# Performance work log

Hardware: AMD Instinct MI355X
Metric: run time of the kernel (lower is better)

## Reference

```python
import math
import jax, jax.numpy as jnp
import numpy as np

N_HEADS = 16
NUM_BUCKETS = 32
MAX_DISTANCE = 128


def _relative_position_bucket(relative_positions, num_buckets=NUM_BUCKETS, max_distance=MAX_DISTANCE):
    # bidirectional=True branch of the torch helper
    ret = -relative_positions
    nb = num_buckets // 2
    sign = (ret < 0).astype(jnp.int32)
    ret = jnp.abs(ret)
    max_exact = nb // 2
    is_small = ret < max_exact
    # torch .long() truncates toward zero; values in the selected (large) branch are >= 0 so int cast matches
    large = max_exact + jnp.minimum(
        (jnp.log(ret.astype(jnp.float32) / max_exact + 1e-6)
         / math.log(max_distance / max_exact) * (nb - max_exact)).astype(jnp.int32),
        nb - max_exact - 1,
    )
    return jnp.where(is_small, ret, large) + sign * nb


def setup_inputs() -> dict:
    key = jax.random.key(0)
    k1, k2, k3, k4, k5 = jax.random.split(key, 5)
    d_model = 1024
    B, L = 2, 2048
    return {
        "query": jax.random.normal(k1, (B, L, d_model), dtype=jnp.float32),
        "Wq": jax.random.normal(k2, (d_model, d_model), dtype=jnp.float32) * 0.02,
        "Wkv": jax.random.normal(k3, (d_model, 2 * d_model), dtype=jnp.float32) * 0.02,
        "Wo": jax.random.normal(k4, (d_model, d_model), dtype=jnp.float32) * 0.02,
        "rel_bias": jax.random.normal(k5, (N_HEADS * NUM_BUCKETS, 1), dtype=jnp.float32) * 0.02,
    }


def reference(query, Wq, Wkv, Wo, rel_bias):
    B, L, D = query.shape
    H = N_HEADS
    hd = D // H
    scale = 1.0 / math.sqrt(hd)

    q = query @ Wq                      # [B, L, D]
    kv = query @ Wkv                    # [B, L, 2D]
    k, v = jnp.split(kv, 2, axis=-1)

    def split_heads(x):
        return x.reshape(B, L, H, hd).transpose(0, 2, 1, 3)  # [B, H, L, hd]

    q, k, v = map(split_heads, (q, k, v))

    scores = jnp.einsum("bhqd,bhkd->bhqk", q, k) * scale      # [B, H, L, L]

    # relative position bias
    pos = jnp.arange(L)
    rp = pos[None, :] - pos[:, None]                           # mem - ctx, [L, L]
    buckets = _relative_position_bucket(rp)                    # [L, L]
    idx = buckets[None, :, :] + (jnp.arange(H) * NUM_BUCKETS)[:, None, None]  # [H, L, L]
    bias = rel_bias[idx, 0][None]                              # [1, H, L, L]

    attn = jax.nn.softmax(scores + bias, axis=-1)
    out = jnp.einsum("bhqk,bhkd->bhqd", attn, v)               # [B, H, L, hd]
    out = out.transpose(0, 2, 1, 3).reshape(B, L, D) @ Wo      # [B, L, D]
    return out, bias
```

## Files before the change

### kernel.cpp

```cpp
#include <hip/hip_runtime.h>


typedef unsigned short u16;
typedef unsigned int u32;
typedef __attribute__((ext_vector_type(4))) float f32x4;
typedef __attribute__((ext_vector_type(8))) short bf16x8;
typedef __attribute__((ext_vector_type(4))) unsigned short u16x4;

#define MFMA16(a, b, c) __builtin_amdgcn_mfma_f32_16x16x32_bf16(a, b, c, 0, 0, 0)

typedef const __attribute__((address_space(1))) void gvoid;
typedef __attribute__((address_space(3))) void lvoid;
static __device__ __forceinline__ void gll16(const void* g, void* l) {
    __builtin_amdgcn_global_load_lds((gvoid*)g, (lvoid*)l, 16, 0, 0);
}

static __device__ inline u16 f2bf(float f) {
    u32 x = __float_as_uint(f);
    x += 0x7fffu + ((x >> 16) & 1u);
    return (u16)(x >> 16);
}
static __device__ inline u32 pk2(float a, float b) {
    return (u32)f2bf(a) | ((u32)f2bf(b) << 16);
}

__global__ __launch_bounds__(256) void prep(
    const float* __restrict__ X, const float* __restrict__ Wq,
    const float* __restrict__ Wkv, const float* __restrict__ Wo,
    const float* __restrict__ rel_bias, u16* __restrict__ Xb,
    u16* __restrict__ Wt, float* __restrict__ tbl)
{
    __shared__ u16 T[64 * 72];
    const int bx = blockIdx.x, tid = threadIdx.x;
    if (bx < 2048) {
        int i = (bx * 256 + tid) * 8;
        float4 a = *(const float4*)(X + i);
        float4 b = *(const float4*)(X + i + 4);
        uint4 w = { pk2(a.x, a.y), pk2(a.z, a.w), pk2(b.x, b.y), pk2(b.z, b.w) };
        *(uint4*)(Xb + i) = w;
    } else if (bx < 3072) {
        int bx2 = bx - 2048;
        int k0 = (bx2 & 15) * 64;
        int n0 = (bx2 >> 4) * 64;
        const float* src; int ld, nb;
        if (n0 < 1024)      { src = Wq;  ld = 1024; nb = n0; }
        else if (n0 < 3072) { src = Wkv; ld = 2048; nb = n0 - 1024; }
        else                { src = Wo;  ld = 1024; nb = n0 - 3072; }
        const int r0 = tid >> 4, c4 = (tid & 15) * 4;
        for (int rr = 0; rr < 4; rr++) {
            int row = rr * 16 + r0;
            float4 f = *(const float4*)(src + (size_t)(k0 + row) * ld + nb + c4);
            T[(c4 + 0) * 72 + row] = f2bf(f.x);
            T[(c4 + 1) * 72 + row] = f2bf(f.y);
            T[(c4 + 2) * 72 + row] = f2bf(f.z);
            T[(c4 + 3) * 72 + row] = f2bf(f.w);
        }
        __syncthreads();
        const int n = tid >> 2, ks0 = (tid & 3) * 16;
        uint4 u0 = *(const uint4*)&T[n * 72 + ks0];
        uint4 u1 = *(const uint4*)&T[n * 72 + ks0 + 8];
        uint4* d = (uint4*)(Wt + (size_t)(n0 + n) * 1024 + k0 + ks0);
        d[0] = u0; d[1] = u1;
    } else {
        int i = (bx - 3072) * 256 + tid;
        int rel = (i & 4095) - 2047;
        int h = i >> 12;
        int ret = -rel;
        int sign = (ret < 0) ? 1 : 0;
        int aret = (ret < 0) ? -ret : ret;
        int bucket;
        if (aret < 8) {
            bucket = aret;
        } else {
            float v = (logf((float)aret * 0.125f + 1e-6f) / logf(16.0f)) * 8.0f;
            int iv = (int)v;
            bucket = 8 + (iv < 7 ? iv : 7);
        }
        bucket += sign * 16;
        tbl[i] = rel_bias[h * 32 + bucket];
    }
}

__global__ __launch_bounds__(256) void qkv_gemm(
    const u16* __restrict__ Xb, const u16* __restrict__ Wt,
    u16* __restrict__ qws, u16* __restrict__ kws, u16* __restrict__ vtws)
{
    __shared__ u16 As[128 * 64];
    __shared__ u16 Bs[128 * 64];
    const int tid = threadIdx.x;
    const int n0 = blockIdx.x * 128;
    const int m0 = blockIdx.y * 128;
    const int wid = tid >> 6, lane = tid & 63, c = lane & 15, quad = lane >> 4;
    const int wm = (wid >> 1) * 64, wn = (wid & 1) * 64;
    const f32x4 z = {0.f, 0.f, 0.f, 0.f};
    f32x4 acc[4][4];
    for (int i = 0; i < 4; i++) for (int j = 0; j < 4; j++) acc[i][j] = z;
    const int rsub = lane >> 3;
    const int dchunk = (lane & 7) ^ (rsub & 7);
    const u16* ag = Xb + (size_t)(m0 + wid * 32 + rsub) * 1024 + dchunk * 8;
    const u16* bg = Wt + (size_t)(n0 + wid * 32 + rsub) * 1024 + dchunk * 8;
    u16* lA = &As[(wid * 32) * 64];
    u16* lB = &Bs[(wid * 32) * 64];
    const int sw = c & 7;

    for (int kk = 0; kk < 1024; kk += 64) {
        for (int i = 0; i < 4; i++)
            gll16(ag + (size_t)i * 8 * 1024 + kk, lA + i * 8 * 64);
        for (int i = 0; i < 4; i++)
            gll16(bg + (size_t)i * 8 * 1024 + kk, lB + i * 8 * 64);
        __syncthreads();
        for (int ks = 0; ks < 2; ks++) {
            const int sl = ((ks * 4 + quad) ^ sw) * 8;
            bf16x8 af[4], bfr[4];
            for (int im = 0; im < 4; im++)
                af[im] = *(const bf16x8*)&As[(wm + im * 16 + c) * 64 + sl];
            for (int jn = 0; jn < 4; jn++)
                bfr[jn] = *(const bf16x8*)&Bs[(wn + jn * 16 + c) * 64 + sl];
            for (int im = 0; im < 4; im++)
                for (int jn = 0; jn < 4; jn++)
                    acc[im][jn] = MFMA16(af[im], bfr[jn], acc[im][jn]);
        }
        __syncthreads();
    }
    for (int im = 0; im < 4; im++) for (int jn = 0; jn < 4; jn++) {
        int gm0 = m0 + wm + im * 16 + quad * 4;
        int gn = n0 + wn + jn * 16 + c;
        if (gn < 2048) {
            u16* dstbase = (gn < 1024) ? qws : kws;
            int nn = gn & 1023;
            int h = nn >> 6, d = nn & 63;
            for (int r = 0; r < 4; r++) {
                int gm = gm0 + r, bb = gm >> 11, l = gm & 2047;
                dstbase[(((size_t)bb * 16 + h) * 2048 + l) * 64 + d] = f2bf(acc[im][jn][r]);
            }
        } else {
            int nn = gn - 2048;
            int h = nn >> 6, d = nn & 63;
            int bb = gm0 >> 11, l = gm0 & 2047;
            u16x4 pk = { f2bf(acc[im][jn][0]), f2bf(acc[im][jn][1]),
                         f2bf(acc[im][jn][2]), f2bf(acc[im][jn][3]) };
            *(u16x4*)&vtws[(((size_t)bb * 16 + h) * 64 + d) * 2048 + l] = pk;
        }
    }
}

__global__ __launch_bounds__(256, 2) void attn_kernel(
    const u16* __restrict__ qws, const u16* __restrict__ kws,
    const u16* __restrict__ vtws, const float* __restrict__ tbl,
    u16* __restrict__ ows, float* __restrict__ bias_out)
{
    __shared__ u16 QPs[128 * 72];
    __shared__ u16 Ks[2][64 * 72];
    __shared__ u16 Vt[2][64 * 72];
    __shared__ float Bw[2][192];
    const int tid = threadIdx.x;
    const int qt = blockIdx.x, bh = blockIdx.y;
    const int b = bh >> 4, h = bh & 15;
    const u16* qp = qws + (size_t)bh * 2048 * 64;
    const u16* kp = kws + (size_t)bh * 2048 * 64;
    const u16* vp = vtws + (size_t)bh * 64 * 2048;
    const float* tb = tbl + h * 4096;
    const int q0 = qt * 128;
    const int wid = tid >> 6, lane = tid & 63, c = lane & 15, quad = lane >> 4;
    const int qw0 = wid * 32;
    const int srow = tid >> 2, sc0 = (tid & 3) * 16;
    const int birow = tid >> 3, bjj = (tid & 7) * 4;

    {
        int row = tid >> 1, c0 = (tid & 1) * 32;
        const uint4* s = (const uint4*)(qp + (size_t)(q0 + row) * 64 + c0);
        uint4 v0 = s[0], v1 = s[1], v2 = s[2], v3 = s[3];
        uint4* d = (uint4*)&QPs[row * 72 + c0];
        d[0] = v0; d[1] = v1; d[2] = v2; d[3] = v3;
    }
    {
        const uint4* s1 = (const uint4*)(kp + (size_t)srow * 64 + sc0);
        uint4 x0 = s1[0], x1 = s1[1];
        const uint4* s2 = (const uint4*)(vp + (size_t)srow * 2048 + sc0);
        uint4 y0 = s2[0], y1 = s2[1];
        *(uint4*)&Ks[0][srow * 72 + sc0] = x0;
        *(uint4*)&Ks[0][srow * 72 + sc0 + 8] = x1;
        *(uint4*)&Vt[0][srow * 72 + sc0] = y0;
        *(uint4*)&Vt[0][srow * 72 + sc0 + 8] = y1;
        if (tid < 192) Bw[0][tid] = tb[1920 - q0 + tid];
    }
    __syncthreads();
    bf16x8 bq[2][2];
    for (int nt = 0; nt < 2; nt++)
        for (int ks = 0; ks < 2; ks++)
            bq[nt][ks] = *(const bf16x8*)&QPs[(qw0 + nt * 16 + c) * 72 + ks * 32 + quad * 8];
    __syncthreads();
    u16* Ps = QPs + wid * (32 * 72);

    float lrow[2] = { 0.f, 0.f };
    const f32x4 z = {0.f, 0.f, 0.f, 0.f};
    f32x4 accO[2][4];
    for (int i = 0; i < 2; i++) for (int j = 0; j < 4; j++) accO[i][j] = z;

    for (int kt = 0; kt < 32; kt++) {
        const int cur = kt & 1, nxt = cur ^ 1;
        const int k0 = kt * 64;
        uint4 x0, x1, y0, y1; float bwv = 0.f;
        if (kt < 31) {
            const uint4* s1 = (const uint4*)(kp + (size_t)(k0 + 64 + srow) * 64 + sc0);
            x0 = s1[0]; x1 = s1[1];
            const uint4* s2 = (const uint4*)(vp + (size_t)srow * 2048 + k0 + 64 + sc0);
            y0 = s2[0]; y1 = s2[1];
            if (tid < 192) bwv = tb[k0 + 64 - q0 + 1920 + tid];
        }
        f32x4 accS[4][2];
        for (int i = 0; i < 4; i++) { accS[i][0] = z; accS[i][1] = z; }
        for (int ks = 0; ks < 2; ks++)
            for (int ktile = 0; ktile < 4; ktile++) {
                bf16x8 ak = *(const bf16x8*)&Ks[cur][(ktile * 16 + c) * 72 + ks * 32 + quad * 8];
                accS[ktile][0] = MFMA16(ak, bq[0][ks], accS[ktile][0]);
                accS[ktile][1] = MFMA16(ak, bq[1][ks], accS[ktile][1]);
            }
        float rsum[2] = { 0.f, 0.f };
        for (int ktile = 0; ktile < 4; ktile++)
            for (int nt = 0; nt < 2; nt++) {
                const float* bp = &Bw[cur][ktile * 16 + quad * 4 - qw0 - nt * 16 - c + 127];
                float p0 = __expf(fmaf(accS[ktile][nt][0], 0.125f, bp[0]));
                float p1 = __expf(fmaf(accS[ktile][nt][1], 0.125f, bp[1]));
                float p2 = __expf(fmaf(accS[ktile][nt][2], 0.125f, bp[2]));
                float p3 = __expf(fmaf(accS[ktile][nt][3], 0.125f, bp[3]));
                rsum[nt] += (p0 + p1) + (p2 + p3);
                u16x4 pk = { f2bf(p0), f2bf(p1), f2bf(p2), f2bf(p3) };
                *(u16x4*)&Ps[(nt * 16 + c) * 72 + ktile * 16 + quad * 4] = pk;
            }
        lrow[0] += rsum[0]; lrow[1] += rsum[1];
        for (int kb = 0; kb < 2; kb++) {
            bf16x8 bv[4];
            for (int nt = 0; nt < 4; nt++)
                bv[nt] = *(const bf16x8*)&Vt[cur][(nt * 16 + c) * 72 + kb * 32 + quad * 8];
            for (int mt = 0; mt < 2; mt++) {
                bf16x8 ap = *(const bf16x8*)&Ps[(mt * 16 + c) * 72 + kb * 32 + quad * 8];
                for (int nt = 0; nt < 4; nt++)
                    accO[mt][nt] = MFMA16(ap, bv[nt], accO[mt][nt]);
            }
        }
        {
            const int jbase = k0 + b * 32 + bjj;
            const float* tw = tb + (jbase + 2047 - q0);
            float* dstb = bias_out + ((size_t)h * 2048 + q0 + birow) * 2048 + jbase;
            for (int rr = 0; rr < 4; rr++) {
                const float* twp = tw - (birow + rr * 32);
                f32x4 v = { twp[0], twp[1], twp[2], twp[3] };
                __builtin_nontemporal_store(v, (f32x4*)(dstb + (size_t)rr * 32 * 2048));
            }
        }
        if (kt < 31) {
            *(uint4*)&Ks[nxt][srow * 72 + sc0] = x0;
            *(uint4*)&Ks[nxt][srow * 72 + sc0 + 8] = x1;
            *(uint4*)&Vt[nxt][srow * 72 + sc0] = y0;
            *(uint4*)&Vt[nxt][srow * 72 + sc0 + 8] = y1;
            if (tid < 192) Bw[nxt][tid] = bwv;
            __syncthreads();
        }
    }
    for (int nt = 0; nt < 2; nt++) {
        lrow[nt] += __shfl_xor(lrow[nt], 16, 64);
        lrow[nt] += __shfl_xor(lrow[nt], 32, 64);
    }
    for (int mt = 0; mt < 2; mt++)
        for (int r = 0; r < 4; r++) {
            float lq = __shfl(lrow[mt], quad * 4 + r, 64);
            float rl = 1.0f / lq;
            int qg = q0 + qw0 + mt * 16 + quad * 4 + r;
            size_t base = ((size_t)b * 2048 + qg) * 1024 + h * 64;
            for (int nt = 0; nt < 4; nt++)
                ows[base + nt * 16 + c] = f2bf(accO[mt][nt][r] * rl);
        }
}

__global__ __launch_bounds__(256) void out_gemm(
    const u16* __restrict__ O, const u16* __restrict__ Wot, float* __restrict__ out)
{
    __shared__ u16 As[128 * 64];
    __shared__ u16 Bs[128 * 64];
    const int tid = threadIdx.x;
    const int n0 = blockIdx.x * 128;
    const int m0 = blockIdx.y * 128;
    const int wid = tid >> 6, lane = tid & 63, c = lane & 15, quad = lane >> 4;
    const int wm = (wid >> 1) * 64, wn = (wid & 1) * 64;
    const f32x4 z = {0.f, 0.f, 0.f, 0.f};
    f32x4 acc[4][4];
    for (int i = 0; i < 4; i++) for (int j = 0; j < 4; j++) acc[i][j] = z;
    const int rsub = lane >> 3;
    const int dchunk = (lane & 7) ^ (rsub & 7);
    const u16* ag = O + (size_t)(m0 + wid * 32 + rsub) * 1024 + dchunk * 8;
    const u16* bg = Wot + (size_t)(n0 + wid * 32 + rsub) * 1024 + dchunk * 8;
    u16* lA = &As[(wid * 32) * 64];
    u16* lB = &Bs[(wid * 32) * 64];
    const int sw = c & 7;
    for (int kk = 0; kk < 1024; kk += 64) {
        for (int i = 0; i < 4; i++)
            gll16(ag + (size_t)i * 8 * 1024 + kk, lA + i * 8 * 64);
        for (int i = 0; i < 4; i++)
            gll16(bg + (size_t)i * 8 * 1024 + kk, lB + i * 8 * 64);
        __syncthreads();
        for (int ks = 0; ks < 2; ks++) {
            const int sl = ((ks * 4 + quad) ^ sw) * 8;
            bf16x8 af[4], bfr[4];
            for (int im = 0; im < 4; im++)
                af[im] = *(const bf16x8*)&As[(wm + im * 16 + c) * 64 + sl];
            for (int jn = 0; jn < 4; jn++)
                bfr[jn] = *(const bf16x8*)&Bs[(wn + jn * 16 + c) * 64 + sl];
            for (int im = 0; im < 4; im++)
                for (int jn = 0; jn < 4; jn++)
                    acc[im][jn] = MFMA16(af[im], bfr[jn], acc[im][jn]);
        }
        __syncthreads();
    }
    for (int im = 0; im < 4; im++) for (int jn = 0; jn < 4; jn++) {
        int gm0 = m0 + wm + im * 16 + quad * 4;
        int gn = n0 + wn + jn * 16 + c;
        for (int r = 0; r < 4; r++)
            __builtin_nontemporal_store(acc[im][jn][r], &out[(size_t)(gm0 + r) * 1024 + gn]);
    }
}

extern "C" void kernel_launch(void* const* d_in, const int* in_sizes, int n_in,
                              void* d_out, int out_size, void* d_ws, size_t ws_size,
                              hipStream_t stream)
{
    (void)in_sizes; (void)n_in; (void)out_size; (void)ws_size;
    const float* query    = (const float*)d_in[0];
    const float* Wq       = (const float*)d_in[1];
    const float* Wkv      = (const float*)d_in[2];
    const float* Wo       = (const float*)d_in[3];
    const float* rel_bias = (const float*)d_in[4];
    float* out = (float*)d_out;

    float* tbl = (float*)d_ws;
    u16* Xb   = (u16*)((char*)d_ws + 262144);
    u16* Wt   = Xb + 4194304;
    u16* qws  = Wt + 4194304;
    u16* kws  = qws + 4194304;
    u16* vtws = kws + 4194304;
    u16* ows  = vtws + 4194304;

    prep<<<3328, 256, 0, stream>>>(query, Wq, Wkv, Wo, rel_bias, Xb, Wt, tbl);
    qkv_gemm<<<dim3(24, 32), 256, 0, stream>>>(Xb, Wt, qws, kws, vtws);
    attn_kernel<<<dim3(16, 32), 256, 0, stream>>>(qws, kws, vtws, tbl, ows,
                                                  out + 4194304);
    out_gemm<<<dim3(8, 32), 256, 0, stream>>>(ows, Wt + (size_t)3072 * 1024, out);
}
```

Measured before the change: 401.7 us.

## Stage K/V tiles with direct global-to-LDS loads into XOR-swizzled layout

Replaces the register-staged K and V tile prefetch with global_load_lds 16-byte transfers straight into shared memory. The padded row stride of 72 becomes an unpadded stride of 64 with an XOR swizzle on the 8-element chunk index to avoid bank conflicts. The bias tile is premultiplied by log2(e) and the score scale adjusted so exp2f can replace __expf. The aim is to cut VGPR pressure and the register round-trip for prefetch, but it relies on the sync at the end of each iteration to order async LDS writes against reads.

```diff
diff --git a/kernel.cpp b/kernel.cpp
--- a/kernel.cpp
+++ b/kernel.cpp
@@ -150,8 +150,8 @@
     u16* __restrict__ ows, float* __restrict__ bias_out)
 {
     __shared__ u16 QPs[128 * 72];
-    __shared__ u16 Ks[2][64 * 72];
-    __shared__ u16 Vt[2][64 * 72];
+    __shared__ u16 Ks[2][64 * 64];
+    __shared__ u16 Vt[2][64 * 64];
     __shared__ float Bw[2][192];
     const int tid = threadIdx.x;
     const int qt = blockIdx.x, bh = blockIdx.y;
@@ -163,26 +163,28 @@
     const int q0 = qt * 128;
     const int wid = tid >> 6, lane = tid & 63, c = lane & 15, quad = lane >> 4;
     const int qw0 = wid * 32;
-    const int srow = tid >> 2, sc0 = (tid & 3) * 16;
+    const int sw = c & 7;
+    const int rsub = lane >> 3;
+    const int schunk = (lane & 7) ^ rsub;
     const int birow = tid >> 3, bjj = (tid & 7) * 4;
 
+    auto stage = [&](int buf, int k0) {
+        for (int g = 0; g < 2; g++) {
+            gll16(kp + (size_t)(k0 + wid * 16 + g * 8 + rsub) * 64 + schunk * 8,
+                  &Ks[buf][(wid * 16 + g * 8) * 64]);
+            gll16(vp + (size_t)(wid * 16 + g * 8 + rsub) * 2048 + k0 + schunk * 8,
+                  &Vt[buf][(wid * 16 + g * 8) * 64]);
+        }
+        if (tid < 192) Bw[buf][tid] = tb[k0 - q0 + 1920 + tid] * 1.44269504f;
+    };
+
+    stage(0, 0);
     {
         int row = tid >> 1, c0 = (tid & 1) * 32;
         const uint4* s = (const uint4*)(qp + (size_t)(q0 + row) * 64 + c0);
         uint4 v0 = s[0], v1 = s[1], v2 = s[2], v3 = s[3];
         uint4* d = (uint4*)&QPs[row * 72 + c0];
         d[0] = v0; d[1] = v1; d[2] = v2; d[3] = v3;
-    }
-    {
-        const uint4* s1 = (const uint4*)(kp + (size_t)srow * 64 + sc0);
-        uint4 x0 = s1[0], x1 = s1[1];
-        const uint4* s2 = (const uint4*)(vp + (size_t)srow * 2048 + sc0);
-        uint4 y0 = s2[0], y1 = s2[1];
-        *(uint4*)&Ks[0][srow * 72 + sc0] = x0;
-        *(uint4*)&Ks[0][srow * 72 + sc0 + 8] = x1;
-        *(uint4*)&Vt[0][srow * 72 + sc0] = y0;
-        *(uint4*)&Vt[0][srow * 72 + sc0 + 8] = y1;
-        if (tid < 192) Bw[0][tid] = tb[1920 - q0 + tid];
     }
     __syncthreads();
     bf16x8 bq[2][2];
@@ -198,21 +200,15 @@
     for (int i = 0; i < 2; i++) for (int j = 0; j < 4; j++) accO[i][j] = z;
 
     for (int kt = 0; kt < 32; kt++) {
-        const int cur = kt & 1, nxt = cur ^ 1;
+        const int cur = kt & 1;
         const int k0 = kt * 64;
-        uint4 x0, x1, y0, y1; float bwv = 0.f;
-        if (kt < 31) {
-            const uint4* s1 = (const uint4*)(kp + (size_t)(k0 + 64 + srow) * 64 + sc0);
-            x0 = s1[0]; x1 = s1[1];
-            const uint4* s2 = (const uint4*)(vp + (size_t)srow * 2048 + k0 + 64 + sc0);
-            y0 = s2[0]; y1 = s2[1];
-            if (tid < 192) bwv = tb[k0 + 64 - q0 + 1920 + tid];
-        }
+        if (kt < 31) stage(cur ^ 1, k0 + 64);
         f32x4 accS[4][2];
         for (int i = 0; i < 4; i++) { accS[i][0] = z; accS[i][1] = z; }
         for (int ks = 0; ks < 2; ks++)
             for (int ktile = 0; ktile < 4; ktile++) {
-                bf16x8 ak = *(const bf16x8*)&Ks[cur][(ktile * 16 + c) * 72 + ks * 32 + quad * 8];
+                bf16x8 ak = *(const bf16x8*)
+                    &Ks[cur][(ktile * 16 + c) * 64 + (((ks * 4 + quad) ^ sw)) * 8];
                 accS[ktile][0] = MFMA16(ak, bq[0][ks], accS[ktile][0]);
                 accS[ktile][1] = MFMA16(ak, bq[1][ks], accS[ktile][1]);
             }
@@ -220,10 +216,10 @@
         for (int ktile = 0; ktile < 4; ktile++)
             for (int nt = 0; nt < 2; nt++) {
                 const float* bp = &Bw[cur][ktile * 16 + quad * 4 - qw0 - nt * 16 - c + 127];
-                float p0 = __expf(fmaf(accS[ktile][nt][0], 0.125f, bp[0]));
-                float p1 = __expf(fmaf(accS[ktile][nt][1], 0.125f, bp[1]));
-                float p2 = __expf(fmaf(accS[ktile][nt][2], 0.125f, bp[2]));
-                float p3 = __expf(fmaf(accS[ktile][nt][3], 0.125f, bp[3]));
+                float p0 = exp2f(fmaf(accS[ktile][nt][0], 0.180336878f, bp[0]));
+                float p1 = exp2f(fmaf(accS[ktile][nt][1], 0.180336878f, bp[1]));
+                float p2 = exp2f(fmaf(accS[ktile][nt][2], 0.180336878f, bp[2]));
+                float p3 = exp2f(fmaf(accS[ktile][nt][3], 0.180336878f, bp[3]));
                 rsum[nt] += (p0 + p1) + (p2 + p3);
                 u16x4 pk = { f2bf(p0), f2bf(p1), f2bf(p2), f2bf(p3) };
                 *(u16x4*)&Ps[(nt * 16 + c) * 72 + ktile * 16 + quad * 4] = pk;
@@ -232,7 +228,8 @@
         for (int kb = 0; kb < 2; kb++) {
             bf16x8 bv[4];
             for (int nt = 0; nt < 4; nt++)
-                bv[nt] = *(const bf16x8*)&Vt[cur][(nt * 16 + c) * 72 + kb * 32 + quad * 8];
+                bv[nt] = *(const bf16x8*)
+                    &Vt[cur][(nt * 16 + c) * 64 + (((kb * 4 + quad) ^ sw)) * 8];
             for (int mt = 0; mt < 2; mt++) {
                 bf16x8 ap = *(const bf16x8*)&Ps[(mt * 16 + c) * 72 + kb * 32 + quad * 8];
                 for (int nt = 0; nt < 4; nt++)
@@ -249,14 +246,7 @@
                 __builtin_nontemporal_store(v, (f32x4*)(dstb + (size_t)rr * 32 * 2048));
             }
         }
-        if (kt < 31) {
-            *(uint4*)&Ks[nxt][srow * 72 + sc0] = x0;
-            *(uint4*)&Ks[nxt][srow * 72 + sc0 + 8] = x1;
-            *(uint4*)&Vt[nxt][srow * 72 + sc0] = y0;
-            *(uint4*)&Vt[nxt][srow * 72 + sc0 + 8] = y1;
-            if (tid < 192) Bw[nxt][tid] = bwv;
-            __syncthreads();
-        }
+        __syncthreads();
     }
     for (int nt = 0; nt < 2; nt++) {
         lrow[nt] += __shfl_xor(lrow[nt], 16, 64);
```

Result: no change. 405.6 us (+1.0%).

## Split bias tensor writes between QKV GEMM and attention; use exp2 softmax

Applied to the files above, without the earlier changes.

Half of the large relative-position bias output (alternate 64-column groups) is now written by the QKV GEMM kernel, interleaved with its K loop, so those stores overlap GEMM compute. The attention kernel writes only the remaining half. The softmax switches from expf to exp2f by pre-scaling the bias and the score scale by log2(e), which removes a multiply per exponent. The risk is extra memory traffic contending with the GEMM's global-to-LDS loads. A no-op change to the swizzle expression is also included.

```diff
diff --git a/kernel.cpp b/kernel.cpp
--- a/kernel.cpp
+++ b/kernel.cpp
@@ -83,7 +83,8 @@
 
 __global__ __launch_bounds__(256) void qkv_gemm(
     const u16* __restrict__ Xb, const u16* __restrict__ Wt,
-    u16* __restrict__ qws, u16* __restrict__ kws, u16* __restrict__ vtws)
+    u16* __restrict__ qws, u16* __restrict__ kws, u16* __restrict__ vtws,
+    const float* __restrict__ tbl, float* __restrict__ bias_out)
 {
     __shared__ u16 As[128 * 64];
     __shared__ u16 Bs[128 * 64];
@@ -96,14 +97,16 @@
     f32x4 acc[4][4];
     for (int i = 0; i < 4; i++) for (int j = 0; j < 4; j++) acc[i][j] = z;
     const int rsub = lane >> 3;
-    const int dchunk = (lane & 7) ^ (rsub & 7);
+    const int dchunk = (lane & 7) ^ rsub;
     const u16* ag = Xb + (size_t)(m0 + wid * 32 + rsub) * 1024 + dchunk * 8;
     const u16* bg = Wt + (size_t)(n0 + wid * 32 + rsub) * 1024 + dchunk * 8;
     u16* lA = &As[(wid * 32) * 64];
     u16* lB = &Bs[(wid * 32) * 64];
     const int sw = c & 7;
-
-    for (int kk = 0; kk < 1024; kk += 64) {
+    const u32 bl = blockIdx.y * 24 + blockIdx.x;
+
+    for (int it = 0; it < 16; it++) {
+        const int kk = it * 64;
         for (int i = 0; i < 4; i++)
             gll16(ag + (size_t)i * 8 * 1024 + kk, lA + i * 8 * 64);
         for (int i = 0; i < 4; i++)
@@ -119,6 +122,22 @@
             for (int im = 0; im < 4; im++)
                 for (int jn = 0; jn < 4; jn++)
                     acc[im][jn] = MFMA16(af[im], bfr[jn], acc[im][jn]);
+        }
+        {
+            const u32 fbase = ((bl * 16 + (u32)it) * 256 + (u32)tid) * 3;
+            for (u32 t = 0; t < 3; t++) {
+                u32 f = fbase + t;
+                if (f < 8388608u) {
+                    u32 r = f >> 8, o = f & 255u;
+                    u32 p = o >> 4, q = o & 15u;
+                    int j = (int)(128u * p + 64u + 4u * q);
+                    int h = (int)(r >> 11), i = (int)(r & 2047u);
+                    const float* s = tbl + h * 4096 + (j - i + 2047);
+                    f32x4 v = { s[0], s[1], s[2], s[3] };
+                    __builtin_nontemporal_store(
+                        v, (f32x4*)(bias_out + ((size_t)r << 11) + j));
+                }
+            }
         }
         __syncthreads();
     }
@@ -182,7 +201,7 @@
         *(uint4*)&Ks[0][srow * 72 + sc0 + 8] = x1;
         *(uint4*)&Vt[0][srow * 72 + sc0] = y0;
         *(uint4*)&Vt[0][srow * 72 + sc0 + 8] = y1;
-        if (tid < 192) Bw[0][tid] = tb[1920 - q0 + tid];
+        if (tid < 192) Bw[0][tid] = tb[1920 - q0 + tid] * 1.44269504f;
     }
     __syncthreads();
     bf16x8 bq[2][2];
@@ -220,10 +239,10 @@
         for (int ktile = 0; ktile < 4; ktile++)
             for (int nt = 0; nt < 2; nt++) {
                 const float* bp = &Bw[cur][ktile * 16 + quad * 4 - qw0 - nt * 16 - c + 127];
-                float p0 = __expf(fmaf(accS[ktile][nt][0], 0.125f, bp[0]));
-                float p1 = __expf(fmaf(accS[ktile][nt][1], 0.125f, bp[1]));
-                float p2 = __expf(fmaf(accS[ktile][nt][2], 0.125f, bp[2]));
-                float p3 = __expf(fmaf(accS[ktile][nt][3], 0.125f, bp[3]));
+                float p0 = exp2f(fmaf(accS[ktile][nt][0], 0.180336878f, bp[0]));
+                float p1 = exp2f(fmaf(accS[ktile][nt][1], 0.180336878f, bp[1]));
+                float p2 = exp2f(fmaf(accS[ktile][nt][2], 0.180336878f, bp[2]));
+                float p3 = exp2f(fmaf(accS[ktile][nt][3], 0.180336878f, bp[3]));
                 rsum[nt] += (p0 + p1) + (p2 + p3);
                 u16x4 pk = { f2bf(p0), f2bf(p1), f2bf(p2), f2bf(p3) };
                 *(u16x4*)&Ps[(nt * 16 + c) * 72 + ktile * 16 + quad * 4] = pk;
@@ -239,7 +258,7 @@
                     accO[mt][nt] = MFMA16(ap, bv[nt], accO[mt][nt]);
             }
         }
-        {
+        if ((kt & 1) == 0) {
             const int jbase = k0 + b * 32 + bjj;
             const float* tw = tb + (jbase + 2047 - q0);
             float* dstb = bias_out + ((size_t)h * 2048 + q0 + birow) * 2048 + jbase;
@@ -254,7 +273,7 @@
             *(uint4*)&Ks[nxt][srow * 72 + sc0 + 8] = x1;
             *(uint4*)&Vt[nxt][srow * 72 + sc0] = y0;
             *(uint4*)&Vt[nxt][srow * 72 + sc0 + 8] = y1;
-            if (tid < 192) Bw[nxt][tid] = bwv;
+            if (tid < 192) Bw[nxt][tid] = bwv * 1.44269504f;
             __syncthreads();
         }
     }
@@ -287,7 +306,7 @@
     f32x4 acc[4][4];
     for (int i = 0; i < 4; i++) for (int j = 0; j < 4; j++) acc[i][j] = z;
     const int rsub = lane >> 3;
-    const int dchunk = (lane & 7) ^ (rsub & 7);
+    const int dchunk = (lane & 7) ^ rsub;
     const u16* ag = O + (size_t)(m0 + wid * 32 + rsub) * 1024 + dchunk * 8;
     const u16* bg = Wot + (size_t)(n0 + wid * 32 + rsub) * 1024 + dchunk * 8;
     u16* lA = &As[(wid * 32) * 64];
@@ -341,7 +360,8 @@
     u16* ows  = vtws + 4194304;
 
     prep<<<3328, 256, 0, stream>>>(query, Wq, Wkv, Wo, rel_bias, Xb, Wt, tbl);
-    qkv_gemm<<<dim3(24, 32), 256, 0, stream>>>(Xb, Wt, qws, kws, vtws);
+    qkv_gemm<<<dim3(24, 32), 256, 0, stream>>>(Xb, Wt, qws, kws, vtws,
+                                               tbl, out + 4194304);
     attn_kernel<<<dim3(16, 32), 256, 0, stream>>>(qws, kws, vtws, tbl, ows,
                                                   out + 4194304);
     out_gemm<<<dim3(8, 32), 256, 0, stream>>>(ows, Wt + (size_t)3072 * 1024, out);
```

After: 535.1 us. 33.2% more time.
